# Optimization experiments

Measured on AMD Instinct MI355X. Metric: run time of the kernel, lower is better.

The kernel has to match this reference:

```python
import jax, jax.numpy as jnp
import numpy as np
from jax import lax

# Module hyperparameters (from DBScan.__init__ defaults, dim per ctor)
EPS = 0.12
MIN_PTS = 10
NUM_CLASSES = 5
DIM = 3
N_POINTS = 8192
N_COLS = DIM + 1 + 1 + NUM_CLASSES  # coords + batch_index + feature + seg logits


def setup_inputs() -> dict:
    key = jax.random.key(0)
    x = jax.random.uniform(key, (N_POINTS, N_COLS), dtype=jnp.float32)
    return {"x": x}


def _dbscan_labels(coords, class_idx):
    """Vectorized DBSCAN equivalent to the sequential region-query/BFS version.

    Cluster = connected component of core points under the eps-graph (restricted
    to points of the same semantic class); border points join the lowest-id
    cluster among their core neighbors (matching the sequential scan order).
    Cluster ids are numbered globally by (class_id, min core index), which
    matches the seed order of the sequential algorithm and the order in which
    clusters are emitted by the original forward.
    Returns int32 labels of shape (N,), noise = -1.
    """
    N = coords.shape[0]
    SENT = N  # sentinel > any valid index
    idx = jnp.arange(N)

    # pairwise squared distances via gram trick: d2 = |a|^2 + |b|^2 - 2 a.b
    sq = jnp.sum(coords * coords, axis=1)
    d2 = sq[:, None] + sq[None, :] - 2.0 * (coords @ coords.T)  # [N, N]
    same_class = class_idx[:, None] == class_idx[None, :]
    adj = (d2 < EPS * EPS) & same_class            # eps-neighborhood (incl. self)
    core = jnp.sum(adj, axis=1) >= MIN_PTS          # core points
    adj_core = adj & core[None, :]                  # edges into core neighbors

    # min-label propagation over the core-core graph (converges to min core
    # index of each connected component)
    comp0 = jnp.where(core, idx, SENT)

    def step(comp):
        nb_min = jnp.min(jnp.where(adj_core, comp[None, :], SENT), axis=1)
        return jnp.where(core, jnp.minimum(comp, nb_min), SENT)

    def cond_fn(carry):
        return carry[1]

    def body_fn(carry):
        comp, _ = carry
        new = step(comp)
        return new, jnp.any(new != comp)

    comp, _ = lax.while_loop(cond_fn, body_fn, (comp0, jnp.array(True)))

    # border points: non-core with at least one core neighbor -> min root among
    # core neighbors (== lowest cluster id, matching sequential absorption)
    nb_root = jnp.min(jnp.where(adj_core, comp[None, :], SENT), axis=1)
    point_root = jnp.where(core, comp, nb_root)     # SENT -> noise
    clustered = point_root < SENT

    # renumber roots globally by (class_id, root index)
    is_root = core & (comp == idx)
    BIG = jnp.int32(N * (NUM_CLASSES + 2))
    sort_key = jnp.where(is_root, class_idx.astype(jnp.int32) * N + idx.astype(jnp.int32), BIG)
    order = jnp.argsort(sort_key)
    rank = jnp.zeros((N,), jnp.int32).at[order].set(jnp.arange(N, dtype=jnp.int32))
    safe_root = jnp.minimum(point_root, N - 1)
    labels = jnp.where(clustered, rank[safe_root], jnp.int32(-1))
    return labels


def reference(x):
    coords = lax.stop_gradient(x[:, :DIM])
    seg = x[:, -NUM_CLASSES:]
    class_idx = jnp.argmax(lax.stop_gradient(seg), axis=1)
    labels = _dbscan_labels(coords, class_idx)
    clustered = labels >= 0
    data = x[:, :-NUM_CLASSES]                       # (N, DIM+2)
    # per-point row of the original's padded cluster output: [data, class_id];
    # noise points are zeroed (they are dropped by the original forward)
    out = jnp.where(clustered[:, None],
                    jnp.concatenate([data, class_idx.astype(x.dtype)[:, None]], axis=1),
                    jnp.zeros((), x.dtype))
    return out, labels
```

## Files before the change

### kernel.cpp

```cpp
#include <hip/hip_runtime.h>
#include <hip/hip_bf16.h>

#define N        8192
#define W        128
#define NCLS     5
#define NCOLS    10
#define MIN_PTS  10
#define EPS2     0.0144f
#define SENT     N
#define NREG     64
#define CAP      8192
#define MAXO     (1 << 20)
#define TILE     2048

__device__ float4             g_pts[N];
__device__ int                g_cls[N];
__device__ int                g_deg[N];
__device__ int                g_parent[N];
__device__ int                g_pointroot[N];
__device__ int                g_rootlabel[N];
__device__ unsigned long long g_adj[N * W];
__device__ unsigned long long g_coremask[W];
__device__ int                g_rc64[NREG * 32];
__device__ int2               g_e64[NREG * CAP];
__device__ int                g_ecnt;
__device__ int2               g_oedges[MAXO];

__global__ void k_setup(const float* __restrict__ x) {
    int i = blockIdx.x * blockDim.x + threadIdx.x;
    if (i >= N) return;
    const float* r = x + i * NCOLS;
    float c0 = r[0], c1 = r[1], c2 = r[2];
    float best = r[5]; int bi = 0;
#pragma unroll
    for (int c = 1; c < NCLS; ++c) {
        float v = r[5 + c];
        if (v > best) { best = v; bi = c; }
    }
    float sq = __fadd_rn(__fadd_rn(__fmul_rn(c0, c0), __fmul_rn(c1, c1)), __fmul_rn(c2, c2));
    g_pts[i] = make_float4(c0, c1, c2, sq);
    g_cls[i] = bi;
    g_pointroot[i] = SENT;
    if (i < NREG * 32) g_rc64[i] = 0;
    if (i == 0) g_ecnt = 0;
}

__global__ void __launch_bounds__(256) k_adj() {
    __shared__ float4 s_pts[TILE];
    __shared__ int    s_cls[TILE];
    int wave = threadIdx.x >> 6;
    int lane = threadIdx.x & 63;
    int i0 = (blockIdx.x * 4 + wave) * 4;
    float4 pA = g_pts[i0 + 0], pB = g_pts[i0 + 1], pC = g_pts[i0 + 2], pD = g_pts[i0 + 3];
    int    cA = g_cls[i0 + 0], cB = g_cls[i0 + 1], cC = g_cls[i0 + 2], cD = g_cls[i0 + 3];
    int    dA = 0, dB = 0, dC = 0, dD = 0;
    for (int tile = 0; tile < N; tile += TILE) {
        for (int k = threadIdx.x; k < TILE; k += 256) {
            s_pts[k] = g_pts[tile + k];
            s_cls[k] = g_cls[tile + k];
        }
        __syncthreads();
        int wbase = tile >> 6;
#pragma unroll 2
        for (int w = 0; w < TILE / 64; ++w) {
            float4 q = s_pts[(w << 6) + lane];
            int   cj = s_cls[(w << 6) + lane];
#define ADJ_ROW(P, CI, DI)                                                      \
            {                                                                   \
                float dot = __builtin_fmaf(P.z, q.z,                            \
                            __builtin_fmaf(P.y, q.y,                            \
                            __builtin_fmaf(P.x, q.x, 0.0f)));                   \
                float d2v = (P.w + q.w) - 2.0f * dot;                           \
                bool adjb = (d2v < EPS2) && (CI == cj);                         \
                unsigned long long word = __ballot(adjb);                       \
                if (lane == (DI)) {                                             \
                    g_adj[(size_t)(i0 + (DI)) * W + wbase + w] = word;          \
                }                                                               \
                if (lane == 0) {                                                \
                    (DI) == 0 ? dA += __popcll(word) :                          \
                    (DI) == 1 ? dB += __popcll(word) :                          \
                    (DI) == 2 ? dC += __popcll(word) : (dD += __popcll(word));  \
                }                                                               \
            }
            ADJ_ROW(pA, cA, 0)
            ADJ_ROW(pB, cB, 1)
            ADJ_ROW(pC, cC, 2)
            ADJ_ROW(pD, cD, 3)
#undef ADJ_ROW
        }
        __syncthreads();
    }
    if (lane == 0) {
        g_deg[i0 + 0] = dA; g_deg[i0 + 1] = dB;
        g_deg[i0 + 2] = dC; g_deg[i0 + 3] = dD;
    }
}

__global__ void k_core() {
    int i = blockIdx.x * blockDim.x + threadIdx.x;
    bool c = g_deg[i] >= MIN_PTS;
    unsigned long long m = __ballot(c);
    if ((threadIdx.x & 63) == 0) g_coremask[i >> 6] = m;
}

__global__ void k_edges() {
    __shared__ unsigned long long s_core[W];
    int t = threadIdx.x;
    if (t < W) s_core[t] = g_coremask[t];
    __syncthreads();
    int gid = blockIdx.x * blockDim.x + t;
    int i = gid >> 7, w = gid & 127;
    int jbase = w << 6;
    unsigned long long word = 0ull;
    if (jbase < i && ((s_core[i >> 6] >> (i & 63)) & 1)) {
        word = g_adj[i * W + w] & s_core[w];
        int lim = i - jbase;
        if (lim < 64) word &= (1ull << lim) - 1;
    }
    int cnt = __popcll(word);
    int lane = t & 63;
    int pre = cnt;
#pragma unroll
    for (int d = 1; d < 64; d <<= 1) {
        int v = __shfl_up(pre, d);
        if (lane >= d) pre += v;
    }
    int total = __shfl(pre, 63);
    if (total == 0) return;
    int r = (gid >> 6) & (NREG - 1);
    int base = 0;
    if (lane == 63) base = atomicAdd(&g_rc64[r * 32], total);
    base = __shfl(base, 63);
    int off = base + pre - cnt;
    while (word) {
        int k = __builtin_ctzll(word);
        word &= word - 1;
        if (off < CAP) {
            g_e64[r * CAP + off] = make_int2(i, jbase + k);
        } else {
            int o = atomicAdd(&g_ecnt, 1);
            if (o < MAXO) g_oedges[o] = make_int2(i, jbase + k);
        }
        ++off;
    }
}

__global__ void __launch_bounds__(1024) k_cc() {
    __shared__ int sp[N];
    __shared__ unsigned int s_rm[NCLS][W * 2];
    __shared__ unsigned long long s_core[W];
    int t = threadIdx.x;
    for (int i = t; i < N; i += 1024) sp[i] = i;
    for (int i = t; i < NCLS * W * 2; i += 1024) ((unsigned int*)s_rm)[i] = 0u;
    if (t < W) s_core[t] = g_coremask[t];
    __syncthreads();
    volatile int* vsp = sp;

    auto unite = [&](int ra, int rb) {
        for (;;) {
            for (;;) {
                int p = vsp[ra];
                if (p == ra) break;
                int gp = vsp[p];
                if (gp != p) vsp[ra] = gp;
                ra = gp;
            }
            for (;;) {
                int p = vsp[rb];
                if (p == rb) break;
                int gp = vsp[p];
                if (gp != p) vsp[rb] = gp;
                rb = gp;
            }
            if (ra == rb) return;
            int hi = ra > rb ? ra : rb;
            int lo = ra < rb ? ra : rb;
            int old = atomicCAS(&sp[hi], hi, lo);
            if (old == hi) return;
            ra = old; rb = lo;
        }
    };

    int wid = t >> 6, lane = t & 63;
#pragma unroll
    for (int rr = 0; rr < NREG / 16; ++rr) {
        int r = wid * (NREG / 16) + rr;
        int cnt = g_rc64[r * 32];
        if (cnt > CAP) cnt = CAP;
        for (int e = lane; e < cnt; e += 64) {
            int2 ed = g_e64[r * CAP + e];
            unite(ed.x, ed.y);
        }
    }
    int ocnt = g_ecnt; if (ocnt > MAXO) ocnt = MAXO;
    for (int e = t; e < ocnt; e += 1024) {
        int2 ed = g_oedges[e];
        unite(ed.x, ed.y);
    }
    __syncthreads();
    for (int i = t; i < N; i += 1024) {
        int r = i, p = sp[r];
        while (p != r) { r = p; p = sp[r]; }
        g_parent[i] = r;
        bool corei = (s_core[i >> 6] >> (i & 63)) & 1;
        if (corei && r == i)
            atomicOr(&s_rm[g_cls[i]][i >> 5], 1u << (i & 31));
    }
    __syncthreads();
    for (int i = t; i < N; i += 1024) {
        bool corei = (s_core[i >> 6] >> (i & 63)) & 1;
        if (!corei || g_parent[i] != i) continue;
        int c = g_cls[i];
        int cnt = 0;
        for (int cc = 0; cc < c; ++cc)
            for (int w = 0; w < W * 2; ++w) cnt += __popc(s_rm[cc][w]);
        int wi = i >> 5;
        for (int w = 0; w < wi; ++w) cnt += __popc(s_rm[c][w]);
        cnt += __popc(s_rm[c][wi] & ((1u << (i & 31)) - 1u));
        g_rootlabel[i] = cnt;
    }
}

__global__ void k_pointroot() {
    __shared__ unsigned long long s_core[W];
    int t = threadIdx.x;
    if (t < W) s_core[t] = g_coremask[t];
    __syncthreads();
    int gid = blockIdx.x * blockDim.x + t;
    int i = gid >> 7, w = gid & 127;
    bool corei = (s_core[i >> 6] >> (i & 63)) & 1;
    if (corei) {
        if (w == 0) g_pointroot[i] = g_parent[i];
        return;
    }
    unsigned long long word = g_adj[i * W + w] & s_core[w];
    if (!word) return;
    int m = SENT;
    while (word) {
        int k = __builtin_ctzll(word);
        word &= word - 1;
        int r = g_parent[(w << 6) + k];
        m = m < r ? m : r;
    }
    atomicMin(&g_pointroot[i], m);
}

__global__ void k_output(const float* __restrict__ x, float* __restrict__ out) {
    int i = blockIdx.x * blockDim.x + threadIdx.x;
    if (i >= N) return;
    int pr = g_pointroot[i];
    bool clustered = (pr < SENT);
    float o[6] = {0.f, 0.f, 0.f, 0.f, 0.f, 0.f};
    float lab = -1.0f;
    if (clustered) {
        lab = (float)g_rootlabel[pr];
        const float* r = x + i * NCOLS;
#pragma unroll
        for (int k = 0; k < 5; ++k) o[k] = r[k];
        o[5] = (float)g_cls[i];
    }
    float* orow = out + i * 6;
#pragma unroll
    for (int k = 0; k < 6; ++k) orow[k] = o[k];
    out[N * 6 + i] = lab;
}

extern "C" void kernel_launch(void* const* d_in, const int* in_sizes, int n_in,
                              void* d_out, int out_size, void* d_ws, size_t ws_size,
                              hipStream_t stream) {
    const float* x = (const float*)d_in[0];
    float* out = (float*)d_out;
    (void)in_sizes; (void)n_in; (void)out_size; (void)d_ws; (void)ws_size;

    k_setup    <<<N / 256, 256, 0, stream>>>(x);
    k_adj      <<<N / 16,  256, 0, stream>>>();
    k_core     <<<N / 256, 256, 0, stream>>>();
    k_edges    <<<(N * W) / 256, 256, 0, stream>>>();
    k_cc       <<<1, 1024, 0, stream>>>();
    k_pointroot<<<(N * W) / 256, 256, 0, stream>>>();
    k_output   <<<N / 256, 256, 0, stream>>>(x, out);
}
```

Baseline: 177.6 us.

## Replace union-find with iterative hook-and-shortcut label propagation in CC kernel

```diff
diff --git a/kernel.cpp b/kernel.cpp
--- a/kernel.cpp
+++ b/kernel.cpp
@@ -149,58 +149,50 @@
     __shared__ int sp[N];
     __shared__ unsigned int s_rm[NCLS][W * 2];
     __shared__ unsigned long long s_core[W];
+    __shared__ int s_cnt[NREG];
+    __shared__ int s_changed;
     int t = threadIdx.x;
     for (int i = t; i < N; i += 1024) sp[i] = i;
     for (int i = t; i < NCLS * W * 2; i += 1024) ((unsigned int*)s_rm)[i] = 0u;
     if (t < W) s_core[t] = g_coremask[t];
+    if (t < NREG) {
+        int c = g_rc64[t * 32];
+        s_cnt[t] = c < CAP ? c : CAP;
+    }
     __syncthreads();
     volatile int* vsp = sp;
-
-    auto unite = [&](int ra, int rb) {
-        for (;;) {
-            for (;;) {
-                int p = vsp[ra];
-                if (p == ra) break;
-                int gp = vsp[p];
-                if (gp != p) vsp[ra] = gp;
-                ra = gp;
+    int ocnt = g_ecnt; if (ocnt > MAXO) ocnt = MAXO;
+
+    for (;;) {
+        if (t == 0) s_changed = 0;
+        __syncthreads();
+        int ch = 0;
+        for (int r = 0; r < NREG; ++r) {
+            int cnt = s_cnt[r];
+            for (int e = t; e < cnt; e += 1024) {
+                int2 ed = g_e64[r * CAP + e];
+                int u = vsp[ed.x], v = vsp[ed.y];
+                if (u < v)      { int old = atomicMin(&sp[v], u); if (old > u) ch = 1; }
+                else if (v < u) { int old = atomicMin(&sp[u], v); if (old > v) ch = 1; }
             }
-            for (;;) {
-                int p = vsp[rb];
-                if (p == rb) break;
-                int gp = vsp[p];
-                if (gp != p) vsp[rb] = gp;
-                rb = gp;
-            }
-            if (ra == rb) return;
-            int hi = ra > rb ? ra : rb;
-            int lo = ra < rb ? ra : rb;
-            int old = atomicCAS(&sp[hi], hi, lo);
-            if (old == hi) return;
-            ra = old; rb = lo;
-        }
-    };
-
-    int wid = t >> 6, lane = t & 63;
-#pragma unroll
-    for (int rr = 0; rr < NREG / 16; ++rr) {
-        int r = wid * (NREG / 16) + rr;
-        int cnt = g_rc64[r * 32];
-        if (cnt > CAP) cnt = CAP;
-        for (int e = lane; e < cnt; e += 64) {
-            int2 ed = g_e64[r * CAP + e];
-            unite(ed.x, ed.y);
-        }
-    }
-    int ocnt = g_ecnt; if (ocnt > MAXO) ocnt = MAXO;
-    for (int e = t; e < ocnt; e += 1024) {
-        int2 ed = g_oedges[e];
-        unite(ed.x, ed.y);
-    }
-    __syncthreads();
+        }
+        for (int e = t; e < ocnt; e += 1024) {
+            int2 ed = g_oedges[e];
+            int u = vsp[ed.x], v = vsp[ed.y];
+            if (u < v)      { int old = atomicMin(&sp[v], u); if (old > u) ch = 1; }
+            else if (v < u) { int old = atomicMin(&sp[u], v); if (old > v) ch = 1; }
+        }
+        __syncthreads();
+        for (int i = t; i < N; i += 1024) {
+            int p = vsp[i], gp = vsp[p];
+            if (gp != p) { sp[i] = gp; ch = 1; }
+        }
+        if (ch) s_changed = 1;
+        __syncthreads();
+        if (!s_changed) break;
+    }
     for (int i = t; i < N; i += 1024) {
-        int r = i, p = sp[r];
-        while (p != r) { r = p; p = sp[r]; }
+        int r = sp[i];
         g_parent[i] = r;
         bool corei = (s_core[i >> 6] >> (i & 63)) & 1;
         if (corei && r == i)
@@ -209,7 +201,7 @@
     __syncthreads();
     for (int i = t; i < N; i += 1024) {
         bool corei = (s_core[i >> 6] >> (i & 63)) & 1;
-        if (!corei || g_parent[i] != i) continue;
+        if (!corei || sp[i] != i) continue;
         int c = g_cls[i];
         int cnt = 0;
         for (int cc = 0; cc < c; ++cc)
```

Measured after the change: 231.4 us. +30.3%, slower.
